# Kernel tuning notes

Hardware: AMD Instinct MI355X
Metric: run time of the kernel (lower is better)

Reference implementation:

```python
import jax, jax.numpy as jnp
import numpy as np

D = 64
H = 256


def _directions(d):
    """Taylor-coefficient directions matching Bilaplacian._set_up_taylor_coefficients."""
    eye = np.eye(d, dtype=np.float32)
    dirs1 = 4.0 * eye                                   # (D, D): 4*e_i
    pairs_neq = np.array([(i, j) for i in range(d) for j in range(d) if i != j])
    dirs2 = 3.0 * eye[pairs_neq[:, 0]] + eye[pairs_neq[:, 1]]      # (D(D-1), D): 3 e_i + e_j
    pairs_lt = np.array([(i, j) for i in range(d) for j in range(i + 1, d)])
    dirs3 = 2.0 * eye[pairs_lt[:, 0]] + 2.0 * eye[pairs_lt[:, 1]]  # (D(D-1)/2, D): 2 e_i + 2 e_j
    return jnp.asarray(dirs1), jnp.asarray(dirs2), jnp.asarray(dirs3)


def setup_inputs() -> dict:
    key = jax.random.key(0)
    ks = jax.random.split(key, 7)
    x = jax.random.normal(ks[0], (D,), dtype=jnp.float32)
    W1 = jax.random.normal(ks[1], (H, D), dtype=jnp.float32) / np.sqrt(D)
    b1 = 0.1 * jax.random.normal(ks[2], (H,), dtype=jnp.float32)
    W2 = jax.random.normal(ks[3], (H, H), dtype=jnp.float32) / np.sqrt(H)
    b2 = 0.1 * jax.random.normal(ks[4], (H,), dtype=jnp.float32)
    W3 = jax.random.normal(ks[5], (1, H), dtype=jnp.float32) / np.sqrt(H)
    b3 = 0.1 * jax.random.normal(ks[6], (1,), dtype=jnp.float32)
    return {"x": x, "W1": W1, "b1": b1, "W2": W2, "b2": b2, "W3": W3, "b3": b3}


def _bilaplacian(x, W1, b1, W2, b2, W3, b3):
    d = x.shape[0]

    def f(z):
        h = jnp.tanh(W1 @ z + b1)
        h = jnp.tanh(W2 @ h + b2)
        return W3 @ h + b3  # (1,)

    def d4(v):
        # 4th directional derivative d^4/dt^4 f(x + t v) via Taylor-mode (nested jvp)
        g1 = lambda z: jax.jvp(f, (z,), (v,))[1]
        g2 = lambda z: jax.jvp(g1, (z,), (v,))[1]
        g3 = lambda z: jax.jvp(g2, (z,), (v,))[1]
        return jax.jvp(g3, (x,), (v,))[1]

    dirs1, dirs2, dirs3 = _directions(d)
    S1 = jax.vmap(d4)(dirs1).sum(0)
    S2 = jax.vmap(d4)(dirs2).sum(0)
    S3 = jax.vmap(d4)(dirs3).sum(0)
    # Polarization weights s.t. alpha*S1 + beta*S2 + gamma*S3 = sum_{i,j} d^4 f / dx_i^2 dx_j^2
    alpha = (1.0 + 13.0 * (d - 1) / 9.0) / 256.0
    beta = -1.0 / 36.0
    gamma = 5.0 / 96.0
    return alpha * S1 + beta * S2 + gamma * S3


def reference(x, W1, b1, W2, b2, W3, b3):
    return _bilaplacian(x, W1, b1, W2, b2, W3, b3)
```

## Files before the change

kernel.cpp:

```cpp
#include <hip/hip_runtime.h>
#include <hip/hip_bf16.h>


#define C_F    0
#define R2_F   1280
#define E_F    1536
#define Q_F    2560
#define S5_F   2816
#define P2_F   3072
#define UP_F   3328
#define S3P_F  4352
#define S4P_F  5376
#define G_F    6400
#define P_F    71936

__global__ __launch_bounds__(256) void k1_kernel(
    const float* __restrict__ x,  const float* __restrict__ W1,
    const float* __restrict__ b1, const float* __restrict__ W2,
    const float* __restrict__ b2, const float* __restrict__ W3,
    float* __restrict__ ws_f, int* __restrict__ cnt) {
    __shared__ __align__(16) float smem[8704];
    int tid = threadIdx.x, b = blockIdx.x;

    if (b < 16) {
        int nb = b >> 2, pb = b & 3;
        float* As = smem;
        float* Bs = smem + 4352;
        for (int idx = tid; idx < 4096; idx += 256) {
            int r = idx >> 6, i = idx & 63;
            As[i * 68 + r] = W1[(nb * 64 + r) * 64 + i];
            Bs[i * 68 + r] = W1[(pb * 64 + r) * 64 + i];
        }
        __syncthreads();
        int r0 = (tid & 15) * 4, c0 = (tid >> 4) * 4;
        float a[4][4] = {};
        for (int i = 0; i < 64; i++) {
            float4 av = *(const float4*)&As[i * 68 + r0];
            float4 bv = *(const float4*)&Bs[i * 68 + c0];
            float ar[4] = {av.x, av.y, av.z, av.w};
            float br[4] = {bv.x, bv.y, bv.z, bv.w};
            #pragma unroll
            for (int rr = 0; rr < 4; rr++)
                #pragma unroll
                for (int cc = 0; cc < 4; cc++)
                    a[rr][cc] = fmaf(ar[rr], br[cc], a[rr][cc]);
        }
        float* G = ws_f + G_F;
        #pragma unroll
        for (int rr = 0; rr < 4; rr++)
            #pragma unroll
            for (int cc = 0; cc < 4; cc++)
                G[(nb * 64 + r0 + rr) * 256 + pb * 64 + c0 + cc] = a[rr][cc];
    } else if (b < 24) {
        int m0 = (b - 16) * 32;
        float* Wc  = smem;
        float* Bc  = smem + 2176;
        float* c1s = smem + 6528;
        float* xs  = smem + 6784;
        if (tid < 64) xs[tid] = x[tid];
        __syncthreads();
        {
            const float4* row = (const float4*)(W1 + tid * 64);
            const float4* xv4 = (const float4*)xs;
            float u0 = b1[tid];
            #pragma unroll
            for (int k = 0; k < 16; k++) {
                float4 w = row[k], xv = xv4[k];
                u0 += w.x * xv.x + w.y * xv.y + w.z * xv.z + w.w * xv.w;
            }
            float T = tanhf(u0);
            c1s[tid] = 1.f - T * T;
        }
        float acc2[2][4] = {};
        int tm2 = (tid & 15) * 2, ti = (tid >> 4) * 4;
        for (int nc = 0; nc < 4; nc++) {
            __syncthreads();
            for (int idx = tid; idx < 2048; idx += 256) {
                int mm = idx >> 6, nn = idx & 63;
                Wc[nn * 34 + mm] = W2[(m0 + mm) * 256 + nc * 64 + nn];
            }
            for (int idx = tid; idx < 4096; idx += 256) {
                int nn = idx >> 6, ii = idx & 63, n = nc * 64 + nn;
                Bc[nn * 68 + ii] = c1s[n] * W1[n * 64 + ii];
            }
            __syncthreads();
            for (int nn = 0; nn < 64; nn++) {
                float2 a2 = *(const float2*)&Wc[nn * 34 + tm2];
                float4 b4 = *(const float4*)&Bc[nn * 68 + ti];
                float br[4] = {b4.x, b4.y, b4.z, b4.w};
                #pragma unroll
                for (int j = 0; j < 4; j++) {
                    acc2[0][j] = fmaf(a2.x, br[j], acc2[0][j]);
                    acc2[1][j] = fmaf(a2.y, br[j], acc2[1][j]);
                }
            }
        }
        float* P = ws_f + P_F;
        float s0 = 0.f, s1 = 0.f;
        #pragma unroll
        for (int j = 0; j < 4; j++) {
            P[(m0 + tm2) * 64 + ti + j]     = acc2[0][j];
            P[(m0 + tm2 + 1) * 64 + ti + j] = acc2[1][j];
            s0 += acc2[0][j] * acc2[0][j];
            s1 += acc2[1][j] * acc2[1][j];
        }
        __syncthreads();
        float* red = smem;
        red[tm2 * 16 + (tid >> 4)]       = s0;
        red[(tm2 + 1) * 16 + (tid >> 4)] = s1;
        __syncthreads();
        if (tid < 32) {
            float p = 0.f;
            #pragma unroll
            for (int g = 0; g < 16; g++) p += red[tid * 16 + g];
            ws_f[P2_F + m0 + tid] = p;
        }
    } else if (b < 28) {
        int m0 = (b - 24) * 64;
        float* Ws   = smem;
        float* h0s  = smem + 4160;
        float* aqs  = smem + 4416;
        float* a5s  = smem + 4672;
        float* part = smem + 4928;
        float* xs   = smem + 5696;
        if (tid < 64) xs[tid] = x[tid];
        __syncthreads();
        {
            const float4* row = (const float4*)(W1 + tid * 64);
            const float4* xv4 = (const float4*)xs;
            float u0 = b1[tid], r2v = 0.f;
            #pragma unroll
            for (int k = 0; k < 16; k++) {
                float4 w = row[k], xv = xv4[k];
                u0  += w.x * xv.x + w.y * xv.y + w.z * xv.z + w.w * xv.w;
                r2v += w.x * w.x + w.y * w.y + w.z * w.z + w.w * w.w;
            }
            float T = tanhf(u0), s = 1.f - T * T;
            float c2 = -2.f * T * s;
            float c4 = s * T * (16.f - 24.f * T * T);
            h0s[tid] = T;
            aqs[tid] = c2 * r2v;
            a5s[tid] = c4 * r2v * r2v;
        }
        int mm = tid & 63, nq = tid >> 6;
        float pv = 0.f, pq = 0.f, p5 = 0.f;
        for (int nc = 0; nc < 4; nc++) {
            __syncthreads();
            for (int idx = tid; idx < 4096; idx += 256) {
                int m2 = idx >> 6, nn = idx & 63;
                Ws[nn * 65 + m2] = W2[(m0 + m2) * 256 + nc * 64 + nn];
            }
            __syncthreads();
            #pragma unroll
            for (int k = 0; k < 16; k++) {
                int nn = nq * 16 + k, n = nc * 64 + nn;
                float wv = Ws[nn * 65 + mm];
                pv = fmaf(wv, h0s[n], pv);
                pq = fmaf(wv, aqs[n], pq);
                p5 = fmaf(wv, a5s[n], p5);
            }
        }
        part[nq * 64 + mm]       = pv;
        part[256 + nq * 64 + mm] = pq;
        part[512 + nq * 64 + mm] = p5;
        __syncthreads();
        if (tid < 64) {
            int m = m0 + tid;
            float v  = b2[m] + part[tid] + part[64 + tid] + part[128 + tid] + part[192 + tid];
            float q  = part[256 + tid] + part[320 + tid] + part[384 + tid] + part[448 + tid];
            float s5 = part[512 + tid] + part[576 + tid] + part[640 + tid] + part[704 + tid];
            float T2 = tanhf(v), s2 = 1.f - T2 * T2, w3 = W3[m];
            float* E = ws_f + E_F;
            E[m]       = w3 * s2;
            E[256 + m] = -2.f * w3 * T2 * s2;
            E[512 + m] = w3 * s2 * (6.f * T2 * T2 - 2.f);
            E[768 + m] = w3 * s2 * T2 * (16.f - 24.f * T2 * T2);
            ws_f[Q_F + m]  = q;
            ws_f[S5_F + m] = s5;
        }
    } else {
        float* xs = smem;
        if (tid < 64) xs[tid] = x[tid];
        __syncthreads();
        const float4* row = (const float4*)(W1 + tid * 64);
        const float4* xv4 = (const float4*)xs;
        float u0 = b1[tid], r2v = 0.f;
        #pragma unroll
        for (int k = 0; k < 16; k++) {
            float4 w = row[k], xv = xv4[k];
            u0  += w.x * xv.x + w.y * xv.y + w.z * xv.z + w.w * xv.w;
            r2v += w.x * w.x + w.y * w.y + w.z * w.z + w.w * w.w;
        }
        float T = tanhf(u0), s = 1.f - T * T;
        ws_f[C_F + tid]       = s;
        ws_f[C_F + 256 + tid] = -2.f * T * s;
        ws_f[C_F + 512 + tid] = s * (6.f * T * T - 2.f);
        ws_f[C_F + 768 + tid] = s * T * (16.f - 24.f * T * T);
        ws_f[R2_F + tid] = r2v;
        if (tid == 0) *cnt = 0;
    }
}

__global__ __launch_bounds__(256) void k2_kernel(
    const float* __restrict__ W1, const float* __restrict__ W2,
    float* __restrict__ ws_f, int* __restrict__ cnt, float* __restrict__ out) {
    __shared__ __align__(16) float smem[13248];
    __shared__ int lastFlag;
    __shared__ double dsum[4];
    int tid = threadIdx.x, b = blockIdx.x;

    if (b < 16) {
        int kb = b >> 2, mb = b & 3;
        const float* c2g = ws_f + C_F + 256;
        float* As  = smem;
        float* Bs  = smem + 4352;
        float* W2k = smem + 8704;
        float* c2k = smem + 13056;
        for (int idx = tid; idx < 4096; idx += 256) {
            int a_ = idx >> 6, b_ = idx & 63;
            W2k[a_ * 68 + b_] = W2[(mb * 64 + a_) * 256 + kb * 64 + b_];
        }
        if (tid < 64) c2k[tid] = c2g[kb * 64 + tid];
        int r0 = (tid & 15) * 4, c0 = (tid >> 4) * 4;
        float a[4][4] = {};
        const float* G = ws_f + G_F;
        for (int nc = 0; nc < 4; nc++) {
            __syncthreads();
            float c2v = c2g[nc * 64 + (tid & 63)];
            for (int idx = tid; idx < 4096; idx += 256) {
                int a_ = idx >> 6, b_ = idx & 63;
                float gv = G[(kb * 64 + a_) * 256 + nc * 64 + b_];
                As[b_ * 68 + a_] = c2v * gv * gv;
                Bs[b_ * 68 + a_] = W2[(mb * 64 + a_) * 256 + nc * 64 + b_];
            }
            __syncthreads();
            for (int nn = 0; nn < 64; nn++) {
                float4 av = *(const float4*)&As[nn * 68 + r0];
                float4 bv = *(const float4*)&Bs[nn * 68 + c0];
                float ar[4] = {av.x, av.y, av.z, av.w};
                float br[4] = {bv.x, bv.y, bv.z, bv.w};
                #pragma unroll
                for (int rr = 0; rr < 4; rr++)
                    #pragma unroll
                    for (int cc = 0; cc < 4; cc++)
                        a[rr][cc] = fmaf(ar[rr], br[cc], a[rr][cc]);
            }
        }
        #pragma unroll
        for (int cc = 0; cc < 4; cc++) {
            float up = 0.f;
            #pragma unroll
            for (int rr = 0; rr < 4; rr++)
                up += a[rr][cc] * c2k[r0 + rr] * W2k[(c0 + cc) * 68 + r0 + rr];
            up += __shfl_xor(up, 8, 16);
            up += __shfl_xor(up, 4, 16);
            up += __shfl_xor(up, 2, 16);
            up += __shfl_xor(up, 1, 16);
            if ((tid & 15) == 0)
                ws_f[UP_F + kb * 256 + mb * 64 + c0 + cc] = up;
        }
    } else {
        int tb = b - 16, mb = tb >> 2, nb = tb & 3;
        float* As  = smem;
        float* Bs  = smem + 4352;
        float* W2s = smem + 8704;
        float* c2s = smem + 13056;
        float* c34 = smem + 13120;
        const float* P = ws_f + P_F;
        for (int idx = tid; idx < 4096; idx += 256) {
            int a_ = idx >> 6, b_ = idx & 63;
            As[b_ * 68 + a_]  = P[(mb * 64 + a_) * 64 + b_];
            Bs[b_ * 68 + a_]  = W1[(nb * 64 + a_) * 64 + b_];
            W2s[a_ * 68 + b_] = W2[(mb * 64 + a_) * 256 + nb * 64 + b_];
        }
        if (tid < 64) {
            int n = nb * 64 + tid;
            c2s[tid] = ws_f[C_F + 256 + n];
            c34[tid] = ws_f[C_F + 512 + n] * ws_f[R2_F + n];
        }
        __syncthreads();
        int m0t = (tid >> 4) * 4, n0t = (tid & 15) * 4;
        float a[4][4] = {};
        for (int ii = 0; ii < 64; ii++) {
            float4 av = *(const float4*)&As[ii * 68 + m0t];
            float4 bv = *(const float4*)&Bs[ii * 68 + n0t];
            float ar[4] = {av.x, av.y, av.z, av.w};
            float br[4] = {bv.x, bv.y, bv.z, bv.w};
            #pragma unroll
            for (int rr = 0; rr < 4; rr++)
                #pragma unroll
                for (int cc = 0; cc < 4; cc++)
                    a[rr][cc] = fmaf(ar[rr], br[cc], a[rr][cc]);
        }
        #pragma unroll
        for (int rr = 0; rr < 4; rr++) {
            float s3p = 0.f, s4p = 0.f;
            #pragma unroll
            for (int cc = 0; cc < 4; cc++) {
                float wv = W2s[(m0t + rr) * 68 + n0t + cc];
                float t  = a[rr][cc];
                s3p = fmaf(c2s[n0t + cc] * wv, t * t, s3p);
                s4p = fmaf(c34[n0t + cc] * wv, t, s4p);
            }
            s3p += __shfl_xor(s3p, 8, 16); s4p += __shfl_xor(s4p, 8, 16);
            s3p += __shfl_xor(s3p, 4, 16); s4p += __shfl_xor(s4p, 4, 16);
            s3p += __shfl_xor(s3p, 2, 16); s4p += __shfl_xor(s4p, 2, 16);
            s3p += __shfl_xor(s3p, 1, 16); s4p += __shfl_xor(s4p, 1, 16);
            if ((tid & 15) == 0) {
                ws_f[S3P_F + nb * 256 + mb * 64 + m0t + rr] = s3p;
                ws_f[S4P_F + nb * 256 + mb * 64 + m0t + rr] = s4p;
            }
        }
    }

    __threadfence();
    if (tid == 0) lastFlag = (atomicAdd(cnt, 1) == 31) ? 1 : 0;
    __syncthreads();
    if (lastFlag) {
        __threadfence();
        volatile float* wsv = ws_f;
        int m = tid;
        float um  = wsv[UP_F  + m] + wsv[UP_F  + 256 + m] + wsv[UP_F  + 512 + m] + wsv[UP_F  + 768 + m];
        float s3m = wsv[S3P_F + m] + wsv[S3P_F + 256 + m] + wsv[S3P_F + 512 + m] + wsv[S3P_F + 768 + m];
        float s4m = wsv[S4P_F + m] + wsv[S4P_F + 256 + m] + wsv[S4P_F + 512 + m] + wsv[S4P_F + 768 + m];
        float p2 = wsv[P2_F + m], q = wsv[Q_F + m], s5 = wsv[S5_F + m];
        float E1 = wsv[E_F + m], E2 = wsv[E_F + 256 + m];
        float E3 = wsv[E_F + 512 + m], E4 = wsv[E_F + 768 + m];
        float y = E4 * p2 * p2
                + E3 * (2.f * q * p2 + 4.f * s3m)
                + E2 * (q * q + 2.f * um + 4.f * s4m)
                + E1 * s5;
        double part = (double)y;
        for (int off = 32; off > 0; off >>= 1) part += __shfl_down(part, off, 64);
        if ((tid & 63) == 0) dsum[tid >> 6] = part;
        __syncthreads();
        if (tid == 0) out[0] = (float)(dsum[0] + dsum[1] + dsum[2] + dsum[3]);
    }
}

extern "C" void kernel_launch(void* const* d_in, const int* in_sizes, int n_in,
                              void* d_out, int out_size, void* d_ws, size_t ws_size,
                              hipStream_t stream) {
    const float* x  = (const float*)d_in[0];
    const float* W1 = (const float*)d_in[1];
    const float* b1 = (const float*)d_in[2];
    const float* W2 = (const float*)d_in[3];
    const float* b2 = (const float*)d_in[4];
    const float* W3 = (const float*)d_in[5];

    char*  ws   = (char*)d_ws;
    int*   cnt  = (int*)ws;
    float* ws_f = (float*)(ws + 16);
    float* out  = (float*)d_out;

    k1_kernel<<<29, 256, 0, stream>>>(x, W1, b1, W2, b2, W3, ws_f, cnt);
    k2_kernel<<<32, 256, 0, stream>>>(W1, W2, ws_f, cnt, out);
}
```

Measured before the change: 117.8 us.

## Fuse two-kernel pipeline into one kernel with per-block recomputation

```diff
diff --git a/kernel.cpp b/kernel.cpp
--- a/kernel.cpp
+++ b/kernel.cpp
@@ -2,61 +2,31 @@
 #include <hip/hip_bf16.h>
 
 
-#define C_F    0
-#define R2_F   1280
-#define E_F    1536
-#define Q_F    2560
-#define S5_F   2816
-#define P2_F   3072
-#define UP_F   3328
-#define S3P_F  4352
-#define S4P_F  5376
-#define G_F    6400
-#define P_F    71936
-
-__global__ __launch_bounds__(256) void k1_kernel(
+#define E_F    0
+#define Q_F    1024
+#define S5_F   1280
+#define P2_F   1536
+#define UP_F   1792
+#define S3P_F  2816
+#define S4P_F  3840
+
+__global__ __launch_bounds__(256) void fused_kernel(
     const float* __restrict__ x,  const float* __restrict__ W1,
     const float* __restrict__ b1, const float* __restrict__ W2,
     const float* __restrict__ b2, const float* __restrict__ W3,
-    float* __restrict__ ws_f, int* __restrict__ cnt) {
-    __shared__ __align__(16) float smem[8704];
+    float* __restrict__ ws_f, int* __restrict__ cnt, float* __restrict__ out) {
+    __shared__ __align__(16) float smem[13888];
+    __shared__ int lastFlag;
+    __shared__ double dsum[4];
     int tid = threadIdx.x, b = blockIdx.x;
 
     if (b < 16) {
-        int nb = b >> 2, pb = b & 3;
-        float* As = smem;
-        float* Bs = smem + 4352;
-        for (int idx = tid; idx < 4096; idx += 256) {
-            int r = idx >> 6, i = idx & 63;
-            As[i * 68 + r] = W1[(nb * 64 + r) * 64 + i];
-            Bs[i * 68 + r] = W1[(pb * 64 + r) * 64 + i];
-        }
-        __syncthreads();
-        int r0 = (tid & 15) * 4, c0 = (tid >> 4) * 4;
-        float a[4][4] = {};
-        for (int i = 0; i < 64; i++) {
-            float4 av = *(const float4*)&As[i * 68 + r0];
-            float4 bv = *(const float4*)&Bs[i * 68 + c0];
-            float ar[4] = {av.x, av.y, av.z, av.w};
-            float br[4] = {bv.x, bv.y, bv.z, bv.w};
-            #pragma unroll
-            for (int rr = 0; rr < 4; rr++)
-                #pragma unroll
-                for (int cc = 0; cc < 4; cc++)
-                    a[rr][cc] = fmaf(ar[rr], br[cc], a[rr][cc]);
-        }
-        float* G = ws_f + G_F;
-        #pragma unroll
-        for (int rr = 0; rr < 4; rr++)
-            #pragma unroll
-            for (int cc = 0; cc < 4; cc++)
-                G[(nb * 64 + r0 + rr) * 256 + pb * 64 + c0 + cc] = a[rr][cc];
-    } else if (b < 24) {
-        int m0 = (b - 16) * 32;
-        float* Wc  = smem;
-        float* Bc  = smem + 2176;
-        float* c1s = smem + 6528;
-        float* xs  = smem + 6784;
+        int kb = b >> 2, mb = b & 3;
+        float* As  = smem;
+        float* Bs  = smem + 4352;
+        float* Cs  = smem + 8704;
+        float* c2s = smem + 13056;
+        float* xs  = smem + 13312;
         if (tid < 64) xs[tid] = x[tid];
         __syncthreads();
         {
@@ -68,55 +38,193 @@
                 float4 w = row[k], xv = xv4[k];
                 u0 += w.x * xv.x + w.y * xv.y + w.z * xv.z + w.w * xv.w;
             }
-            float T = tanhf(u0);
-            c1s[tid] = 1.f - T * T;
-        }
-        float acc2[2][4] = {};
-        int tm2 = (tid & 15) * 2, ti = (tid >> 4) * 4;
+            float T = tanhf(u0), s = 1.f - T * T;
+            c2s[tid] = -2.f * T * s;
+        }
+        for (int idx = tid; idx < 4096; idx += 256) {
+            int r = idx >> 6, i = idx & 63;
+            As[i * 68 + r] = W1[(kb * 64 + r) * 64 + i];
+        }
+        __syncthreads();
+        int r0 = (tid & 15) * 4, c0 = (tid >> 4) * 4;
+        float acc[4][4] = {};
         for (int nc = 0; nc < 4; nc++) {
-            __syncthreads();
-            for (int idx = tid; idx < 2048; idx += 256) {
-                int mm = idx >> 6, nn = idx & 63;
-                Wc[nn * 34 + mm] = W2[(m0 + mm) * 256 + nc * 64 + nn];
-            }
-            for (int idx = tid; idx < 4096; idx += 256) {
-                int nn = idx >> 6, ii = idx & 63, n = nc * 64 + nn;
-                Bc[nn * 68 + ii] = c1s[n] * W1[n * 64 + ii];
+            for (int idx = tid; idx < 4096; idx += 256) {
+                int r = idx >> 6, i = idx & 63;
+                Bs[i * 68 + r] = W1[(nc * 64 + r) * 64 + i];
+            }
+            __syncthreads();
+            float g[4][4] = {};
+            for (int i = 0; i < 64; i++) {
+                float4 av = *(const float4*)&As[i * 68 + r0];
+                float4 bv = *(const float4*)&Bs[i * 68 + c0];
+                float ar[4] = {av.x, av.y, av.z, av.w};
+                float br[4] = {bv.x, bv.y, bv.z, bv.w};
+                #pragma unroll
+                for (int rr = 0; rr < 4; rr++)
+                    #pragma unroll
+                    for (int cc = 0; cc < 4; cc++)
+                        g[rr][cc] = fmaf(ar[rr], br[cc], g[rr][cc]);
+            }
+            #pragma unroll
+            for (int rr = 0; rr < 4; rr++)
+                #pragma unroll
+                for (int cc = 0; cc < 4; cc++) {
+                    float gv = g[rr][cc];
+                    Cs[(c0 + cc) * 68 + r0 + rr] = c2s[nc * 64 + c0 + cc] * gv * gv;
+                }
+            __syncthreads();
+            for (int idx = tid; idx < 4096; idx += 256) {
+                int a_ = idx >> 6, b_ = idx & 63;
+                Bs[b_ * 68 + a_] = W2[(mb * 64 + a_) * 256 + nc * 64 + b_];
             }
             __syncthreads();
             for (int nn = 0; nn < 64; nn++) {
-                float2 a2 = *(const float2*)&Wc[nn * 34 + tm2];
-                float4 b4 = *(const float4*)&Bc[nn * 68 + ti];
-                float br[4] = {b4.x, b4.y, b4.z, b4.w};
-                #pragma unroll
-                for (int j = 0; j < 4; j++) {
-                    acc2[0][j] = fmaf(a2.x, br[j], acc2[0][j]);
-                    acc2[1][j] = fmaf(a2.y, br[j], acc2[1][j]);
-                }
-            }
-        }
-        float* P = ws_f + P_F;
-        float s0 = 0.f, s1 = 0.f;
+                float4 av = *(const float4*)&Cs[nn * 68 + r0];
+                float4 bv = *(const float4*)&Bs[nn * 68 + c0];
+                float ar[4] = {av.x, av.y, av.z, av.w};
+                float br[4] = {bv.x, bv.y, bv.z, bv.w};
+                #pragma unroll
+                for (int rr = 0; rr < 4; rr++)
+                    #pragma unroll
+                    for (int cc = 0; cc < 4; cc++)
+                        acc[rr][cc] = fmaf(ar[rr], br[cc], acc[rr][cc]);
+            }
+            __syncthreads();
+        }
+        for (int idx = tid; idx < 4096; idx += 256) {
+            int a_ = idx >> 6, b_ = idx & 63;
+            Bs[a_ * 68 + b_] = W2[(mb * 64 + a_) * 256 + kb * 64 + b_];
+        }
+        __syncthreads();
         #pragma unroll
-        for (int j = 0; j < 4; j++) {
-            P[(m0 + tm2) * 64 + ti + j]     = acc2[0][j];
-            P[(m0 + tm2 + 1) * 64 + ti + j] = acc2[1][j];
-            s0 += acc2[0][j] * acc2[0][j];
-            s1 += acc2[1][j] * acc2[1][j];
-        }
-        __syncthreads();
-        float* red = smem;
-        red[tm2 * 16 + (tid >> 4)]       = s0;
-        red[(tm2 + 1) * 16 + (tid >> 4)] = s1;
-        __syncthreads();
-        if (tid < 32) {
-            float p = 0.f;
-            #pragma unroll
-            for (int g = 0; g < 16; g++) p += red[tid * 16 + g];
-            ws_f[P2_F + m0 + tid] = p;
-        }
-    } else if (b < 28) {
-        int m0 = (b - 24) * 64;
+        for (int cc = 0; cc < 4; cc++) {
+            float up = 0.f;
+            #pragma unroll
+            for (int rr = 0; rr < 4; rr++)
+                up += acc[rr][cc] * c2s[kb * 64 + r0 + rr] * Bs[(c0 + cc) * 68 + r0 + rr];
+            up += __shfl_xor(up, 8, 16);
+            up += __shfl_xor(up, 4, 16);
+            up += __shfl_xor(up, 2, 16);
+            up += __shfl_xor(up, 1, 16);
+            if ((tid & 15) == 0)
+                ws_f[UP_F + kb * 256 + mb * 64 + c0 + cc] = up;
+        }
+    } else if (b < 32) {
+        int tb = b - 16, mb = tb >> 2, nb = tb & 3;
+        float* As   = smem;
+        float* Bs2  = smem + 4352;
+        float* Pt   = smem + 8704;
+        float* c1s  = smem + 13056;
+        float* c2v  = smem + 13312;
+        float* c34v = smem + 13568;
+        float* xs   = smem + 13824;
+        if (tid < 64) xs[tid] = x[tid];
+        __syncthreads();
+        {
+            const float4* row = (const float4*)(W1 + tid * 64);
+            const float4* xv4 = (const float4*)xs;
+            float u0 = b1[tid], r2v = 0.f;
+            #pragma unroll
+            for (int k = 0; k < 16; k++) {
+                float4 w = row[k], xv = xv4[k];
+                u0  += w.x * xv.x + w.y * xv.y + w.z * xv.z + w.w * xv.w;
+                r2v += w.x * w.x + w.y * w.y + w.z * w.z + w.w * w.w;
+            }
+            float T = tanhf(u0), s = 1.f - T * T;
+            c1s[tid]  = s;
+            c2v[tid]  = -2.f * T * s;
+            c34v[tid] = s * (6.f * T * T - 2.f) * r2v;
+        }
+        __syncthreads();
+        int r0p = (tid >> 4) * 4, c0p = (tid & 15) * 4;
+        float acc[4][4] = {};
+        for (int nc = 0; nc < 4; nc++) {
+            for (int idx = tid; idx < 4096; idx += 256) {
+                int a_ = idx >> 6, b_ = idx & 63;
+                As[b_ * 68 + a_] = W2[(mb * 64 + a_) * 256 + nc * 64 + b_];
+            }
+            for (int idx = tid; idx < 4096; idx += 256) {
+                int a_ = idx >> 6, b_ = idx & 63;
+                Bs2[a_ * 68 + b_] = c1s[nc * 64 + a_] * W1[(nc * 64 + a_) * 64 + b_];
+            }
+            __syncthreads();
+            for (int nn = 0; nn < 64; nn++) {
+                float4 av = *(const float4*)&As[nn * 68 + r0p];
+                float4 bv = *(const float4*)&Bs2[nn * 68 + c0p];
+                float ar[4] = {av.x, av.y, av.z, av.w};
+                float br[4] = {bv.x, bv.y, bv.z, bv.w};
+                #pragma unroll
+                for (int rr = 0; rr < 4; rr++)
+                    #pragma unroll
+                    for (int cc = 0; cc < 4; cc++)
+                        acc[rr][cc] = fmaf(ar[rr], br[cc], acc[rr][cc]);
+            }
+            __syncthreads();
+        }
+        if (nb == 0) {
+            #pragma unroll
+            for (int rr = 0; rr < 4; rr++) {
+                float p = 0.f;
+                #pragma unroll
+                for (int cc = 0; cc < 4; cc++) p += acc[rr][cc] * acc[rr][cc];
+                p += __shfl_xor(p, 8, 16);
+                p += __shfl_xor(p, 4, 16);
+                p += __shfl_xor(p, 2, 16);
+                p += __shfl_xor(p, 1, 16);
+                if ((tid & 15) == 0)
+                    ws_f[P2_F + mb * 64 + r0p + rr] = p;
+            }
+        }
+        #pragma unroll
+        for (int rr = 0; rr < 4; rr++)
+            #pragma unroll
+            for (int cc = 0; cc < 4; cc++)
+                Pt[(c0p + cc) * 68 + r0p + rr] = acc[rr][cc];
+        __syncthreads();
+        for (int idx = tid; idx < 4096; idx += 256) {
+            int a_ = idx >> 6, b_ = idx & 63;
+            As[b_ * 68 + a_] = W1[(nb * 64 + a_) * 64 + b_];
+        }
+        for (int idx = tid; idx < 4096; idx += 256) {
+            int a_ = idx >> 6, b_ = idx & 63;
+            Bs2[a_ * 68 + b_] = W2[(mb * 64 + a_) * 256 + nb * 64 + b_];
+        }
+        __syncthreads();
+        int m0t = (tid >> 4) * 4, n0t = (tid & 15) * 4;
+        float t4[4][4] = {};
+        for (int ii = 0; ii < 64; ii++) {
+            float4 av = *(const float4*)&Pt[ii * 68 + m0t];
+            float4 bv = *(const float4*)&As[ii * 68 + n0t];
+            float ar[4] = {av.x, av.y, av.z, av.w};
+            float br[4] = {bv.x, bv.y, bv.z, bv.w};
+            #pragma unroll
+            for (int rr = 0; rr < 4; rr++)
+                #pragma unroll
+                for (int cc = 0; cc < 4; cc++)
+                    t4[rr][cc] = fmaf(ar[rr], br[cc], t4[rr][cc]);
+        }
+        #pragma unroll
+        for (int rr = 0; rr < 4; rr++) {
+            float s3p = 0.f, s4p = 0.f;
+            #pragma unroll
+            for (int cc = 0; cc < 4; cc++) {
+                float wv = Bs2[(m0t + rr) * 68 + n0t + cc];
+                float t  = t4[rr][cc];
+                s3p = fmaf(c2v[nb * 64 + n0t + cc] * wv, t * t, s3p);
+                s4p = fmaf(c34v[nb * 64 + n0t + cc] * wv, t, s4p);
+            }
+            s3p += __shfl_xor(s3p, 8, 16); s4p += __shfl_xor(s4p, 8, 16);
+            s3p += __shfl_xor(s3p, 4, 16); s4p += __shfl_xor(s4p, 4, 16);
+            s3p += __shfl_xor(s3p, 2, 16); s4p += __shfl_xor(s4p, 2, 16);
+            s3p += __shfl_xor(s3p, 1, 16); s4p += __shfl_xor(s4p, 1, 16);
+            if ((tid & 15) == 0) {
+                ws_f[S3P_F + nb * 256 + mb * 64 + m0t + rr] = s3p;
+                ws_f[S4P_F + nb * 256 + mb * 64 + m0t + rr] = s4p;
+            }
+        }
+    } else {
+        int m0 = (b - 32) * 64;
         float* Ws   = smem;
         float* h0s  = smem + 4160;
         float* aqs  = smem + 4416;
@@ -170,151 +278,17 @@
             float q  = part[256 + tid] + part[320 + tid] + part[384 + tid] + part[448 + tid];
             float s5 = part[512 + tid] + part[576 + tid] + part[640 + tid] + part[704 + tid];
             float T2 = tanhf(v), s2 = 1.f - T2 * T2, w3 = W3[m];
-            float* E = ws_f + E_F;
-            E[m]       = w3 * s2;
-            E[256 + m] = -2.f * w3 * T2 * s2;
-            E[512 + m] = w3 * s2 * (6.f * T2 * T2 - 2.f);
-            E[768 + m] = w3 * s2 * T2 * (16.f - 24.f * T2 * T2);
+            ws_f[E_F + m]       = w3 * s2;
+            ws_f[E_F + 256 + m] = -2.f * w3 * T2 * s2;
+            ws_f[E_F + 512 + m] = w3 * s2 * (6.f * T2 * T2 - 2.f);
+            ws_f[E_F + 768 + m] = w3 * s2 * T2 * (16.f - 24.f * T2 * T2);
             ws_f[Q_F + m]  = q;
             ws_f[S5_F + m] = s5;
         }
-    } else {
-        float* xs = smem;
-        if (tid < 64) xs[tid] = x[tid];
-        __syncthreads();
-        const float4* row = (const float4*)(W1 + tid * 64);
-        const float4* xv4 = (const float4*)xs;
-        float u0 = b1[tid], r2v = 0.f;
-        #pragma unroll
-        for (int k = 0; k < 16; k++) {
-            float4 w = row[k], xv = xv4[k];
-            u0  += w.x * xv.x + w.y * xv.y + w.z * xv.z + w.w * xv.w;
-            r2v += w.x * w.x + w.y * w.y + w.z * w.z + w.w * w.w;
-        }
-        float T = tanhf(u0), s = 1.f - T * T;
-        ws_f[C_F + tid]       = s;
-        ws_f[C_F + 256 + tid] = -2.f * T * s;
-        ws_f[C_F + 512 + tid] = s * (6.f * T * T - 2.f);
-        ws_f[C_F + 768 + tid] = s * T * (16.f - 24.f * T * T);
-        ws_f[R2_F + tid] = r2v;
-        if (tid == 0) *cnt = 0;
     }
-}
-
-__global__ __launch_bounds__(256) void k2_kernel(
-    const float* __restrict__ W1, const float* __restrict__ W2,
-    float* __restrict__ ws_f, int* __restrict__ cnt, float* __restrict__ out) {
-    __shared__ __align__(16) float smem[13248];
-    __shared__ int lastFlag;
-    __shared__ double dsum[4];
-    int tid = threadIdx.x, b = blockIdx.x;
-
-    if (b < 16) {
-        int kb = b >> 2, mb = b & 3;
-        const float* c2g = ws_f + C_F + 256;
-        float* As  = smem;
-        float* Bs  = smem + 4352;
-        float* W2k = smem + 8704;
-        float* c2k = smem + 13056;
-        for (int idx = tid; idx < 4096; idx += 256) {
-            int a_ = idx >> 6, b_ = idx & 63;
-            W2k[a_ * 68 + b_] = W2[(mb * 64 + a_) * 256 + kb * 64 + b_];
-        }
-        if (tid < 64) c2k[tid] = c2g[kb * 64 + tid];
-        int r0 = (tid & 15) * 4, c0 = (tid >> 4) * 4;
-        float a[4][4] = {};
-        const float* G = ws_f + G_F;
-        for (int nc = 0; nc < 4; nc++) {
-            __syncthreads();
-            float c2v = c2g[nc * 64 + (tid & 63)];
-            for (int idx = tid; idx < 4096; idx += 256) {
-                int a_ = idx >> 6, b_ = idx & 63;
-                float gv = G[(kb * 64 + a_) * 256 + nc * 64 + b_];
-                As[b_ * 68 + a_] = c2v * gv * gv;
-                Bs[b_ * 68 + a_] = W2[(mb * 64 + a_) * 256 + nc * 64 + b_];
-            }
-            __syncthreads();
-            for (int nn = 0; nn < 64; nn++) {
-                float4 av = *(const float4*)&As[nn * 68 + r0];
-                float4 bv = *(const float4*)&Bs[nn * 68 + c0];
-                float ar[4] = {av.x, av.y, av.z, av.w};
-                float br[4] = {bv.x, bv.y, bv.z, bv.w};
-                #pragma unroll
-                for (int rr = 0; rr < 4; rr++)
-                    #pragma unroll
-                    for (int cc = 0; cc < 4; cc++)
-                        a[rr][cc] = fmaf(ar[rr], br[cc], a[rr][cc]);
-            }
-        }
-        #pragma unroll
-        for (int cc = 0; cc < 4; cc++) {
-            float up = 0.f;
-            #pragma unroll
-            for (int rr = 0; rr < 4; rr++)
-                up += a[rr][cc] * c2k[r0 + rr] * W2k[(c0 + cc) * 68 + r0 + rr];
-            up += __shfl_xor(up, 8, 16);
-            up += __shfl_xor(up, 4, 16);
-            up += __shfl_xor(up, 2, 16);
-            up += __shfl_xor(up, 1, 16);
-            if ((tid & 15) == 0)
-                ws_f[UP_F + kb * 256 + mb * 64 + c0 + cc] = up;
-        }
-    } else {
-        int tb = b - 16, mb = tb >> 2, nb = tb & 3;
-        float* As  = smem;
-        float* Bs  = smem + 4352;
-        float* W2s = smem + 8704;
-        float* c2s = smem + 13056;
-        float* c34 = smem + 13120;
-        const float* P = ws_f + P_F;
-        for (int idx = tid; idx < 4096; idx += 256) {
-            int a_ = idx >> 6, b_ = idx & 63;
-            As[b_ * 68 + a_]  = P[(mb * 64 + a_) * 64 + b_];
-            Bs[b_ * 68 + a_]  = W1[(nb * 64 + a_) * 64 + b_];
-            W2s[a_ * 68 + b_] = W2[(mb * 64 + a_) * 256 + nb * 64 + b_];
-        }
-        if (tid < 64) {
-            int n = nb * 64 + tid;
-            c2s[tid] = ws_f[C_F + 256 + n];
-            c34[tid] = ws_f[C_F + 512 + n] * ws_f[R2_F + n];
-        }
-        __syncthreads();
-        int m0t = (tid >> 4) * 4, n0t = (tid & 15) * 4;
-        float a[4][4] = {};
-        for (int ii = 0; ii < 64; ii++) {
-            float4 av = *(const float4*)&As[ii * 68 + m0t];
-            float4 bv = *(const float4*)&Bs[ii * 68 + n0t];
-            float ar[4] = {av.x, av.y, av.z, av.w};
-            float br[4] = {bv.x, bv.y, bv.z, bv.w};
-            #pragma unroll
-            for (int rr = 0; rr < 4; rr++)
-                #pragma unroll
-                for (int cc = 0; cc < 4; cc++)
-                    a[rr][cc] = fmaf(ar[rr], br[cc], a[rr][cc]);
-        }
-        #pragma unroll
-        for (int rr = 0; rr < 4; rr++) {
-            float s3p = 0.f, s4p = 0.f;
-            #pragma unroll
-            for (int cc = 0; cc < 4; cc++) {
-                float wv = W2s[(m0t + rr) * 68 + n0t + cc];
-                float t  = a[rr][cc];
-                s3p = fmaf(c2s[n0t + cc] * wv, t * t, s3p);
-                s4p = fmaf(c34[n0t + cc] * wv, t, s4p);
-            }
-            s3p += __shfl_xor(s3p, 8, 16); s4p += __shfl_xor(s4p, 8, 16);
-            s3p += __shfl_xor(s3p, 4, 16); s4p += __shfl_xor(s4p, 4, 16);
-            s3p += __shfl_xor(s3p, 2, 16); s4p += __shfl_xor(s4p, 2, 16);
-            s3p += __shfl_xor(s3p, 1, 16); s4p += __shfl_xor(s4p, 1, 16);
-            if ((tid & 15) == 0) {
-                ws_f[S3P_F + nb * 256 + mb * 64 + m0t + rr] = s3p;
-                ws_f[S4P_F + nb * 256 + mb * 64 + m0t + rr] = s4p;
-            }
-        }
-    }
 
     __threadfence();
-    if (tid == 0) lastFlag = (atomicAdd(cnt, 1) == 31) ? 1 : 0;
+    if (tid == 0) lastFlag = (atomicAdd(cnt, 1) == 35) ? 1 : 0;
     __syncthreads();
     if (lastFlag) {
         __threadfence();
@@ -353,6 +327,6 @@
     float* ws_f = (float*)(ws + 16);
     float* out  = (float*)d_out;
 
-    k1_kernel<<<29, 256, 0, stream>>>(x, W1, b1, W2, b2, W3, ws_f, cnt);
-    k2_kernel<<<32, 256, 0, stream>>>(W1, W2, ws_f, cnt, out);
+    hipMemsetAsync(ws, 0, 16, stream);
+    fused_kernel<<<36, 256, 0, stream>>>(x, W1, b1, W2, b2, W3, ws_f, cnt, out);
 }
```

After: 108.3 us. -8.1%, faster.

## Split reduction dimension across more blocks in both kernels for higher parallelism

Applied to the files above, without the earlier changes.

```diff
diff --git a/kernel.cpp b/kernel.cpp
--- a/kernel.cpp
+++ b/kernel.cpp
@@ -2,17 +2,16 @@
 #include <hip/hip_bf16.h>
 
 
-#define C_F    0
-#define R2_F   1280
-#define E_F    1536
-#define Q_F    2560
-#define S5_F   2816
-#define P2_F   3072
-#define UP_F   3328
-#define S3P_F  4352
-#define S4P_F  5376
-#define G_F    6400
-#define P_F    71936
+#define E_F    0
+#define Q_F    1024
+#define S5_F   1280
+#define P2_F   1536
+#define CV_F   1792
+#define UP_F   2304
+#define S3P_F  6400
+#define S4P_F  7424
+#define G_F    8448
+#define PP_F   73984
 
 __global__ __launch_bounds__(256) void k1_kernel(
     const float* __restrict__ x,  const float* __restrict__ W1,
@@ -23,13 +22,13 @@
     int tid = threadIdx.x, b = blockIdx.x;
 
     if (b < 16) {
-        int nb = b >> 2, pb = b & 3;
+        int gr = b >> 2, gc = b & 3;
         float* As = smem;
         float* Bs = smem + 4352;
         for (int idx = tid; idx < 4096; idx += 256) {
             int r = idx >> 6, i = idx & 63;
-            As[i * 68 + r] = W1[(nb * 64 + r) * 64 + i];
-            Bs[i * 68 + r] = W1[(pb * 64 + r) * 64 + i];
+            As[i * 68 + r] = W1[(gr * 64 + r) * 64 + i];
+            Bs[i * 68 + r] = W1[(gc * 64 + r) * 64 + i];
         }
         __syncthreads();
         int r0 = (tid & 15) * 4, c0 = (tid >> 4) * 4;
@@ -50,19 +49,20 @@
         for (int rr = 0; rr < 4; rr++)
             #pragma unroll
             for (int cc = 0; cc < 4; cc++)
-                G[(nb * 64 + r0 + rr) * 256 + pb * 64 + c0 + cc] = a[rr][cc];
-    } else if (b < 24) {
-        int m0 = (b - 16) * 32;
+                G[(gr * 64 + r0 + rr) * 256 + gc * 64 + c0 + cc] = a[rr][cc];
+    } else if (b < 48) {
+        int pb = b - 16, mbp = pb >> 2, nc = pb & 3, m0 = mbp * 32;
         float* Wc  = smem;
         float* Bc  = smem + 2176;
         float* c1s = smem + 6528;
-        float* xs  = smem + 6784;
+        float* xs  = smem + 6592;
         if (tid < 64) xs[tid] = x[tid];
         __syncthreads();
-        {
-            const float4* row = (const float4*)(W1 + tid * 64);
+        if (tid < 64) {
+            int n = nc * 64 + tid;
+            const float4* row = (const float4*)(W1 + n * 64);
             const float4* xv4 = (const float4*)xs;
-            float u0 = b1[tid];
+            float u0 = b1[n];
             #pragma unroll
             for (int k = 0; k < 16; k++) {
                 float4 w = row[k], xv = xv4[k];
@@ -71,52 +71,36 @@
             float T = tanhf(u0);
             c1s[tid] = 1.f - T * T;
         }
+        for (int idx = tid; idx < 2048; idx += 256) {
+            int mm = idx >> 6, nn = idx & 63;
+            Wc[nn * 34 + mm] = W2[(m0 + mm) * 256 + nc * 64 + nn];
+        }
+        __syncthreads();
+        for (int idx = tid; idx < 4096; idx += 256) {
+            int nn = idx >> 6, ii = idx & 63;
+            Bc[nn * 68 + ii] = c1s[nn] * W1[(nc * 64 + nn) * 64 + ii];
+        }
+        __syncthreads();
         float acc2[2][4] = {};
         int tm2 = (tid & 15) * 2, ti = (tid >> 4) * 4;
-        for (int nc = 0; nc < 4; nc++) {
-            __syncthreads();
-            for (int idx = tid; idx < 2048; idx += 256) {
-                int mm = idx >> 6, nn = idx & 63;
-                Wc[nn * 34 + mm] = W2[(m0 + mm) * 256 + nc * 64 + nn];
-            }
-            for (int idx = tid; idx < 4096; idx += 256) {
-                int nn = idx >> 6, ii = idx & 63, n = nc * 64 + nn;
-                Bc[nn * 68 + ii] = c1s[n] * W1[n * 64 + ii];
-            }
-            __syncthreads();
-            for (int nn = 0; nn < 64; nn++) {
-                float2 a2 = *(const float2*)&Wc[nn * 34 + tm2];
-                float4 b4 = *(const float4*)&Bc[nn * 68 + ti];
-                float br[4] = {b4.x, b4.y, b4.z, b4.w};
-                #pragma unroll
-                for (int j = 0; j < 4; j++) {
-                    acc2[0][j] = fmaf(a2.x, br[j], acc2[0][j]);
-                    acc2[1][j] = fmaf(a2.y, br[j], acc2[1][j]);
-                }
-            }
-        }
-        float* P = ws_f + P_F;
-        float s0 = 0.f, s1 = 0.f;
+        for (int nn = 0; nn < 64; nn++) {
+            float2 a2 = *(const float2*)&Wc[nn * 34 + tm2];
+            float4 b4 = *(const float4*)&Bc[nn * 68 + ti];
+            float br[4] = {b4.x, b4.y, b4.z, b4.w};
+            #pragma unroll
+            for (int j = 0; j < 4; j++) {
+                acc2[0][j] = fmaf(a2.x, br[j], acc2[0][j]);
+                acc2[1][j] = fmaf(a2.y, br[j], acc2[1][j]);
+            }
+        }
+        float* PPc = ws_f + PP_F + nc * 16384;
         #pragma unroll
         for (int j = 0; j < 4; j++) {
-            P[(m0 + tm2) * 64 + ti + j]     = acc2[0][j];
-            P[(m0 + tm2 + 1) * 64 + ti + j] = acc2[1][j];
-            s0 += acc2[0][j] * acc2[0][j];
-            s1 += acc2[1][j] * acc2[1][j];
-        }
-        __syncthreads();
-        float* red = smem;
-        red[tm2 * 16 + (tid >> 4)]       = s0;
-        red[(tm2 + 1) * 16 + (tid >> 4)] = s1;
-        __syncthreads();
-        if (tid < 32) {
-            float p = 0.f;
-            #pragma unroll
-            for (int g = 0; g < 16; g++) p += red[tid * 16 + g];
-            ws_f[P2_F + m0 + tid] = p;
-        }
-    } else if (b < 28) {
-        int m0 = (b - 24) * 64;
+            PPc[(m0 + tm2) * 64 + ti + j]     = acc2[0][j];
+            PPc[(m0 + tm2 + 1) * 64 + ti + j] = acc2[1][j];
+        }
+    } else if (b < 52) {
+        int m0 = (b - 48) * 64;
         float* Ws   = smem;
         float* h0s  = smem + 4160;
         float* aqs  = smem + 4416;
@@ -170,11 +154,10 @@
             float q  = part[256 + tid] + part[320 + tid] + part[384 + tid] + part[448 + tid];
             float s5 = part[512 + tid] + part[576 + tid] + part[640 + tid] + part[704 + tid];
             float T2 = tanhf(v), s2 = 1.f - T2 * T2, w3 = W3[m];
-            float* E = ws_f + E_F;
-            E[m]       = w3 * s2;
-            E[256 + m] = -2.f * w3 * T2 * s2;
-            E[512 + m] = w3 * s2 * (6.f * T2 * T2 - 2.f);
-            E[768 + m] = w3 * s2 * T2 * (16.f - 24.f * T2 * T2);
+            ws_f[E_F + m]       = w3 * s2;
+            ws_f[E_F + 256 + m] = -2.f * w3 * T2 * s2;
+            ws_f[E_F + 512 + m] = w3 * s2 * (6.f * T2 * T2 - 2.f);
+            ws_f[E_F + 768 + m] = w3 * s2 * T2 * (16.f - 24.f * T2 * T2);
             ws_f[Q_F + m]  = q;
             ws_f[S5_F + m] = s5;
         }
@@ -192,11 +175,8 @@
             r2v += w.x * w.x + w.y * w.y + w.z * w.z + w.w * w.w;
         }
         float T = tanhf(u0), s = 1.f - T * T;
-        ws_f[C_F + tid]       = s;
-        ws_f[C_F + 256 + tid] = -2.f * T * s;
-        ws_f[C_F + 512 + tid] = s * (6.f * T * T - 2.f);
-        ws_f[C_F + 768 + tid] = s * T * (16.f - 24.f * T * T);
-        ws_f[R2_F + tid] = r2v;
+        ws_f[CV_F + tid]       = -2.f * T * s;
+        ws_f[CV_F + 256 + tid] = s * (6.f * T * T - 2.f) * r2v;
         if (tid == 0) *cnt = 0;
     }
 }
@@ -208,89 +188,93 @@
     __shared__ int lastFlag;
     __shared__ double dsum[4];
     int tid = threadIdx.x, b = blockIdx.x;
-
-    if (b < 16) {
-        int kb = b >> 2, mb = b & 3;
-        const float* c2g = ws_f + C_F + 256;
-        float* As  = smem;
+    const float* c2g  = ws_f + CV_F;
+    const float* c34g = ws_f + CV_F + 256;
+
+    if (b < 64) {
+        int kb = b >> 4, mb = (b >> 2) & 3, nc = b & 3;
+        float* Cs  = smem;
         float* Bs  = smem + 4352;
         float* W2k = smem + 8704;
-        float* c2k = smem + 13056;
-        for (int idx = tid; idx < 4096; idx += 256) {
-            int a_ = idx >> 6, b_ = idx & 63;
-            W2k[a_ * 68 + b_] = W2[(mb * 64 + a_) * 256 + kb * 64 + b_];
-        }
-        if (tid < 64) c2k[tid] = c2g[kb * 64 + tid];
+        const float* G = ws_f + G_F;
+        for (int idx = tid; idx < 4096; idx += 256) {
+            int r = idx >> 6, c = idx & 63;
+            float gv = G[(kb * 64 + r) * 256 + nc * 64 + c];
+            Cs[c * 68 + r] = c2g[nc * 64 + c] * gv * gv;
+        }
+        for (int idx = tid; idx < 4096; idx += 256) {
+            int m_ = idx >> 6, n_ = idx & 63;
+            Bs[n_ * 68 + m_] = W2[(mb * 64 + m_) * 256 + nc * 64 + n_];
+        }
+        for (int idx = tid; idx < 4096; idx += 256) {
+            int m_ = idx >> 6, k_ = idx & 63;
+            W2k[m_ * 68 + k_] = W2[(mb * 64 + m_) * 256 + kb * 64 + k_];
+        }
+        __syncthreads();
         int r0 = (tid & 15) * 4, c0 = (tid >> 4) * 4;
         float a[4][4] = {};
-        const float* G = ws_f + G_F;
-        for (int nc = 0; nc < 4; nc++) {
-            __syncthreads();
-            float c2v = c2g[nc * 64 + (tid & 63)];
-            for (int idx = tid; idx < 4096; idx += 256) {
-                int a_ = idx >> 6, b_ = idx & 63;
-                float gv = G[(kb * 64 + a_) * 256 + nc * 64 + b_];
-                As[b_ * 68 + a_] = c2v * gv * gv;
-                Bs[b_ * 68 + a_] = W2[(mb * 64 + a_) * 256 + nc * 64 + b_];
-            }
-            __syncthreads();
-            for (int nn = 0; nn < 64; nn++) {
-                float4 av = *(const float4*)&As[nn * 68 + r0];
-                float4 bv = *(const float4*)&Bs[nn * 68 + c0];
-                float ar[4] = {av.x, av.y, av.z, av.w};
-                float br[4] = {bv.x, bv.y, bv.z, bv.w};
+        for (int nn = 0; nn < 64; nn++) {
+            float4 av = *(const float4*)&Cs[nn * 68 + r0];
+            float4 bv = *(const float4*)&Bs[nn * 68 + c0];
+            float ar[4] = {av.x, av.y, av.z, av.w};
+            float br[4] = {bv.x, bv.y, bv.z, bv.w};
+            #pragma unroll
+            for (int rr = 0; rr < 4; rr++)
                 #pragma unroll
-                for (int rr = 0; rr < 4; rr++)
-                    #pragma unroll
-                    for (int cc = 0; cc < 4; cc++)
-                        a[rr][cc] = fmaf(ar[rr], br[cc], a[rr][cc]);
-            }
+                for (int cc = 0; cc < 4; cc++)
+                    a[rr][cc] = fmaf(ar[rr], br[cc], a[rr][cc]);
         }
         #pragma unroll
         for (int cc = 0; cc < 4; cc++) {
             float up = 0.f;
             #pragma unroll
             for (int rr = 0; rr < 4; rr++)
-                up += a[rr][cc] * c2k[r0 + rr] * W2k[(c0 + cc) * 68 + r0 + rr];
+                up += a[rr][cc] * c2g[kb * 64 + r0 + rr] * W2k[(c0 + cc) * 68 + r0 + rr];
             up += __shfl_xor(up, 8, 16);
             up += __shfl_xor(up, 4, 16);
             up += __shfl_xor(up, 2, 16);
             up += __shfl_xor(up, 1, 16);
             if ((tid & 15) == 0)
-                ws_f[UP_F + kb * 256 + mb * 64 + c0 + cc] = up;
+                ws_f[UP_F + (kb * 4 + nc) * 256 + mb * 64 + c0 + cc] = up;
         }
     } else {
-        int tb = b - 16, mb = tb >> 2, nb = tb & 3;
-        float* As  = smem;
-        float* Bs  = smem + 4352;
-        float* W2s = smem + 8704;
-        float* c2s = smem + 13056;
-        float* c34 = smem + 13120;
-        const float* P = ws_f + P_F;
-        for (int idx = tid; idx < 4096; idx += 256) {
-            int a_ = idx >> 6, b_ = idx & 63;
-            As[b_ * 68 + a_]  = P[(mb * 64 + a_) * 64 + b_];
-            Bs[b_ * 68 + a_]  = W1[(nb * 64 + a_) * 64 + b_];
-            W2s[a_ * 68 + b_] = W2[(mb * 64 + a_) * 256 + nb * 64 + b_];
+        int tb = b - 64, mb = tb >> 2, nb = tb & 3;
+        float* Pt   = smem;
+        float* As   = smem + 4352;
+        float* W2s  = smem + 8704;
+        float* c2s  = smem + 13056;
+        float* c34s = smem + 13120;
+        const float* PP = ws_f + PP_F;
+        for (int idx = tid; idx < 4096; idx += 256) {
+            int ml = idx >> 6, i = idx & 63;
+            int mg = (mb * 64 + ml) * 64 + i;
+            Pt[i * 68 + ml] = PP[mg] + PP[16384 + mg] + PP[32768 + mg] + PP[49152 + mg];
+        }
+        for (int idx = tid; idx < 4096; idx += 256) {
+            int nl = idx >> 6, ii = idx & 63;
+            As[ii * 68 + nl] = W1[(nb * 64 + nl) * 64 + ii];
+        }
+        for (int idx = tid; idx < 4096; idx += 256) {
+            int m_ = idx >> 6, n_ = idx & 63;
+            W2s[m_ * 68 + n_] = W2[(mb * 64 + m_) * 256 + nb * 64 + n_];
         }
         if (tid < 64) {
-            int n = nb * 64 + tid;
-            c2s[tid] = ws_f[C_F + 256 + n];
-            c34[tid] = ws_f[C_F + 512 + n] * ws_f[R2_F + n];
+            c2s[tid]  = c2g[nb * 64 + tid];
+            c34s[tid] = c34g[nb * 64 + tid];
         }
         __syncthreads();
         int m0t = (tid >> 4) * 4, n0t = (tid & 15) * 4;
-        float a[4][4] = {};
+        float t4[4][4] = {};
         for (int ii = 0; ii < 64; ii++) {
-            float4 av = *(const float4*)&As[ii * 68 + m0t];
-            float4 bv = *(const float4*)&Bs[ii * 68 + n0t];
+            float4 av = *(const float4*)&Pt[ii * 68 + m0t];
+            float4 bv = *(const float4*)&As[ii * 68 + n0t];
             float ar[4] = {av.x, av.y, av.z, av.w};
             float br[4] = {bv.x, bv.y, bv.z, bv.w};
             #pragma unroll
             for (int rr = 0; rr < 4; rr++)
                 #pragma unroll
                 for (int cc = 0; cc < 4; cc++)
-                    a[rr][cc] = fmaf(ar[rr], br[cc], a[rr][cc]);
+                    t4[rr][cc] = fmaf(ar[rr], br[cc], t4[rr][cc]);
         }
         #pragma unroll
         for (int rr = 0; rr < 4; rr++) {
@@ -298,9 +282,9 @@
             #pragma unroll
             for (int cc = 0; cc < 4; cc++) {
                 float wv = W2s[(m0t + rr) * 68 + n0t + cc];
-                float t  = a[rr][cc];
+                float t  = t4[rr][cc];
                 s3p = fmaf(c2s[n0t + cc] * wv, t * t, s3p);
-                s4p = fmaf(c34[n0t + cc] * wv, t, s4p);
+                s4p = fmaf(c34s[n0t + cc] * wv, t, s4p);
             }
             s3p += __shfl_xor(s3p, 8, 16); s4p += __shfl_xor(s4p, 8, 16);
             s3p += __shfl_xor(s3p, 4, 16); s4p += __shfl_xor(s4p, 4, 16);
@@ -311,16 +295,26 @@
                 ws_f[S4P_F + nb * 256 + mb * 64 + m0t + rr] = s4p;
             }
         }
+        if (nb == 0 && tid < 64) {
+            float p = 0.f;
+            for (int i = 0; i < 64; i++) {
+                float v = Pt[i * 68 + tid];
+                p = fmaf(v, v, p);
+            }
+            ws_f[P2_F + mb * 64 + tid] = p;
+        }
     }
 
     __threadfence();
-    if (tid == 0) lastFlag = (atomicAdd(cnt, 1) == 31) ? 1 : 0;
+    if (tid == 0) lastFlag = (atomicAdd(cnt, 1) == 79) ? 1 : 0;
     __syncthreads();
     if (lastFlag) {
         __threadfence();
         volatile float* wsv = ws_f;
         int m = tid;
-        float um  = wsv[UP_F  + m] + wsv[UP_F  + 256 + m] + wsv[UP_F  + 512 + m] + wsv[UP_F  + 768 + m];
+        float um = 0.f;
+        #pragma unroll
+        for (int s = 0; s < 16; s++) um += wsv[UP_F + s * 256 + m];
         float s3m = wsv[S3P_F + m] + wsv[S3P_F + 256 + m] + wsv[S3P_F + 512 + m] + wsv[S3P_F + 768 + m];
         float s4m = wsv[S4P_F + m] + wsv[S4P_F + 256 + m] + wsv[S4P_F + 512 + m] + wsv[S4P_F + 768 + m];
         float p2 = wsv[P2_F + m], q = wsv[Q_F + m], s5 = wsv[S5_F + m];
@@ -353,6 +347,6 @@
     float* ws_f = (float*)(ws + 16);
     float* out  = (float*)d_out;
 
-    k1_kernel<<<29, 256, 0, stream>>>(x, W1, b1, W2, b2, W3, ws_f, cnt);
-    k2_kernel<<<32, 256, 0, stream>>>(W1, W2, ws_f, cnt, out);
+    k1_kernel<<<53, 256, 0, stream>>>(x, W1, b1, W2, b2, W3, ws_f, cnt);
+    k2_kernel<<<80, 256, 0, stream>>>(W1, W2, ws_f, cnt, out);
 }
```

Result: faster. 108.2 us (-8.2%).
